# Kernel optimization log

Measured on AMD Instinct MI355X. Metric: run time of the kernel, lower is better.

## Reference

```python
import jax, jax.numpy as jnp
import numpy as np
from functools import partial

N = 50000
IN_C, HID_C, OUT_C = 256, 128, 64
E = 800000


def gcn_norm(src, dst, n_nodes):
    # PyG gcn_norm with unit edge weights: deg from target index, D^-1/2 A D^-1/2
    ones = jnp.ones(src.shape[0], dtype=jnp.float32)
    deg = jax.ops.segment_sum(ones, dst, num_segments=n_nodes)
    dinv = jnp.where(deg > 0, jax.lax.rsqrt(deg), 0.0)
    return dinv[src] * dinv[dst]


def gcn_conv(x, src, dst, norm, W, b):
    h = x @ W                              # [N, out] dense GEMM first (PyG order)
    msg = h[src] * norm[:, None]           # gather + scale  [E', out]
    out = jax.ops.segment_sum(msg, dst, num_segments=x.shape[0])
    return out + b


def setup_inputs() -> dict:
    key = jax.random.key(0)
    ks = jax.random.split(key, 6)
    x = jax.random.normal(ks[0], (N, IN_C), dtype=jnp.float32)
    edge_index = jax.random.randint(ks[1], (2, E), 0, N, dtype=jnp.int32)
    # Glorot-ish init for weights
    W1 = jax.random.normal(ks[2], (IN_C, HID_C), dtype=jnp.float32) / np.sqrt(IN_C)
    b1 = jnp.zeros((HID_C,), dtype=jnp.float32)
    W2 = jax.random.normal(ks[3], (HID_C, OUT_C), dtype=jnp.float32) / np.sqrt(HID_C)
    b2 = jnp.zeros((OUT_C,), dtype=jnp.float32)
    return {"x": x, "edge_index": edge_index, "W1": W1, "b1": b1, "W2": W2, "b2": b2}


def reference(x, edge_index, W1, b1, W2, b2):
    # eval mode: dropout is identity
    n = x.shape[0]
    loop = jnp.arange(n, dtype=edge_index.dtype)
    src = jnp.concatenate([edge_index[0], loop])   # add self loops (static E+N)
    dst = jnp.concatenate([edge_index[1], loop])
    norm = gcn_norm(src, dst, n)
    h = jax.nn.relu(gcn_conv(x, src, dst, norm, W1, b1))
    return gcn_conv(h, src, dst, norm, W2, b2)
```

## Files before the change

### kernel.cpp

```cpp
#include <hip/hip_runtime.h>


#define TPB 256
#define NBKT 196
#define EB_CAP 4608
#define CSR_CAP 6400
#define P1_EPB 4096

typedef __bf16 bf16x8 __attribute__((ext_vector_type(8)));
typedef __bf16 bf16x4 __attribute__((ext_vector_type(4)));
typedef __bf16 bf16x2 __attribute__((ext_vector_type(2)));
typedef float f32x4 __attribute__((ext_vector_type(4)));

__device__ __forceinline__ float bflo(unsigned u) { return __uint_as_float(u << 16); }
__device__ __forceinline__ float bfhi(unsigned u) { return __uint_as_float(u & 0xffff0000u); }

__global__ __launch_bounds__(256) void clear_wprep_kernel(
    unsigned* __restrict__ gcnt, float* __restrict__ dinv, __bf16* __restrict__ h2s,
    int N,
    const float* __restrict__ W1, const float* __restrict__ W2,
    __bf16* __restrict__ wf1, __bf16* __restrict__ wf2) {
    if (blockIdx.x == 0) {
        int t = threadIdx.x;
        if (t < NBKT) gcnt[t] = 0;
        if (t == 0) dinv[N] = 0.0f;
        if (t < 32) ((unsigned*)(h2s + (long)N * 64))[t] = 0u;
        return;
    }
    int g = (blockIdx.x - 1) * TPB + threadIdx.x;
    if (g < 64 * 64) {
        int frag = g >> 6, L = g & 63;
        int kstep = frag >> 3, oct = frag & 7;
        int oc = oct * 16 + (L & 15);
        int k0 = kstep * 32 + (L >> 4) * 8;
        bf16x8 v;
#pragma unroll
        for (int j = 0; j < 8; j++) v[j] = (__bf16)W1[(k0 + j) * 128 + oc];
        ((bf16x8*)wf1)[g] = v;
    } else if (g < 64 * 64 + 16 * 64) {
        int g2 = g - 64 * 64;
        int frag = g2 >> 6, L = g2 & 63;
        int kstep = frag >> 2, oct = frag & 3;
        int oc = oct * 16 + (L & 15);
        int k0 = kstep * 32 + (L >> 4) * 8;
        bf16x8 v;
#pragma unroll
        for (int j = 0; j < 8; j++) v[j] = (__bf16)W2[(k0 + j) * 64 + oc];
        ((bf16x8*)wf2)[g2] = v;
    }
}

__device__ __forceinline__ void gemm1_body(int bid, int tid, const float* __restrict__ x,
                                           const bf16x8* __restrict__ wfrag,
                                           __bf16* __restrict__ outp, int M) {
    int wave = tid >> 6, lane = tid & 63;
    int col = lane & 15, q = lane >> 4;
    long r0 = (long)bid * 64 + wave * 16 + col;
    long r0c = (r0 < M) ? r0 : (M - 1);

    f32x4 acc[8];
#pragma unroll
    for (int o = 0; o < 8; o++) acc[o] = (f32x4){0.f, 0.f, 0.f, 0.f};

#pragma unroll
    for (int ks = 0; ks < 8; ks++) {
        int k0 = ks * 32 + q * 8;
        const float* A0 = x + r0c * 256 + k0;
        float4 f0a = *(const float4*)A0;
        float4 f0b = *(const float4*)(A0 + 4);
        bf16x8 b0;
        b0[0] = (__bf16)f0a.x; b0[1] = (__bf16)f0a.y; b0[2] = (__bf16)f0a.z; b0[3] = (__bf16)f0a.w;
        b0[4] = (__bf16)f0b.x; b0[5] = (__bf16)f0b.y; b0[6] = (__bf16)f0b.z; b0[7] = (__bf16)f0b.w;
#pragma unroll
        for (int ot = 0; ot < 8; ot++) {
            bf16x8 a = wfrag[(ks * 8 + ot) * 64 + lane];
            acc[ot] = __builtin_amdgcn_mfma_f32_16x16x32_bf16(a, b0, acc[ot], 0, 0, 0);
        }
    }

    if (r0 < M) {
#pragma unroll
        for (int ot = 0; ot < 8; ot++) {
            int oc = ot * 16 + q * 4;
            bf16x4 v;
#pragma unroll
            for (int r = 0; r < 4; r++) v[r] = (__bf16)acc[ot][r];
            *(bf16x4*)(outp + r0 * 128 + oc) = v;
        }
    }
}

__global__ __launch_bounds__(256) void p1_gemm1_kernel(
    const int* __restrict__ src, const int* __restrict__ dst, int E, int p1Blocks,
    unsigned* __restrict__ gcnt, unsigned* __restrict__ ebuf,
    const float* __restrict__ x, const bf16x8* __restrict__ wf1,
    __bf16* __restrict__ h1u, int M) {
    __shared__ unsigned sPacked[P1_EPB];
    __shared__ int sCnt[256];
    if ((int)blockIdx.x < p1Blocks) {
        int t = threadIdx.x;
        sCnt[t] = 0;
        __syncthreads();
        long e0 = (long)blockIdx.x * P1_EPB;
        int cnt = (int)(E - e0);
        if (cnt > P1_EPB) cnt = P1_EPB;
        for (int i = t; i < cnt; i += 256) {
            unsigned s = (unsigned)src[e0 + i];
            unsigned d = (unsigned)dst[e0 + i];
            sPacked[i] = (s << 16) | d;
            atomicAdd(&sCnt[d >> 8], 1);
        }
        __syncthreads();
        int base = 0;
        if (t < NBKT) base = (int)atomicAdd(&gcnt[t], (unsigned)sCnt[t]);
        __syncthreads();
        if (t < NBKT) sCnt[t] = t * EB_CAP + base;
        __syncthreads();
        for (int i = t; i < cnt; i += 256) {
            unsigned p = sPacked[i];
            int b = (int)((p & 0xffffu) >> 8);
            int pos = atomicAdd(&sCnt[b], 1);
            if (pos < (b + 1) * EB_CAP) ebuf[pos] = p;
        }
    } else {
        gemm1_body(blockIdx.x - p1Blocks, threadIdx.x, x, wf1, h1u, M);
    }
}

__global__ __launch_bounds__(256) void csr_kernel(
    const unsigned* __restrict__ gcnt, const unsigned* __restrict__ ebuf,
    int* __restrict__ csr, int2* __restrict__ se, float* __restrict__ dinv, int N) {
    __shared__ unsigned sEdges[EB_CAP];
    __shared__ int sCnt[256];
    __shared__ int sScan[256];
    int b = blockIdx.x, t = threadIdx.x;
    int m = (int)gcnt[b];
    if (m > EB_CAP) m = EB_CAP;
    sCnt[t] = 0;
    __syncthreads();
    const unsigned* eb = ebuf + b * EB_CAP;
    for (int i = t; i < m; i += 256) {
        unsigned p = eb[i];
        sEdges[i] = p;
        atomicAdd(&sCnt[p & 255u], 1);
    }
    __syncthreads();
    int c = sCnt[t];
    int pad = (c + 7) & ~7;
    sScan[t] = pad;
    __syncthreads();
    for (int off = 1; off < 256; off <<= 1) {
        int v = (t >= off) ? sScan[t - off] : 0;
        __syncthreads();
        sScan[t] += v;
        __syncthreads();
    }
    int start = b * CSR_CAP + sScan[t] - pad;
    int node = (b << 8) + t;
    if (node < N) {
        se[node] = make_int2(start, start + pad);
        dinv[node] = rsqrtf((float)c + 1.0f);
    }
    __syncthreads();
    sCnt[t] = start;
    __syncthreads();
    for (int i = t; i < m; i += 256) {
        unsigned p = sEdges[i];
        int pos = atomicAdd(&sCnt[p & 255u], 1);
        csr[pos] = (int)(p >> 16);
    }
    if (node < N) {
        for (int k = start + c; k < start + pad; k++) csr[k] = N;
    }
}

#define ACC8()                                             \
    do {                                                   \
        a0x += bflo(v0) * w0; a0y += bfhi(v0) * w0;        \
        a1x += bflo(v1) * w1; a1y += bfhi(v1) * w1;        \
        a2x += bflo(v2) * w2; a2y += bfhi(v2) * w2;        \
        a3x += bflo(v3) * w3; a3y += bfhi(v3) * w3;        \
        a0x += bflo(v4) * w4; a0y += bfhi(v4) * w4;        \
        a1x += bflo(v5) * w5; a1y += bfhi(v5) * w5;        \
        a2x += bflo(v6) * w6; a2y += bfhi(v6) * w6;        \
        a3x += bflo(v7) * w7; a3y += bfhi(v7) * w7;        \
    } while (0)

__global__ __launch_bounds__(256) void agg128_gemm2_kernel(
    const __bf16* __restrict__ h, const int* __restrict__ csr,
    const int2* __restrict__ se, const float* __restrict__ dinv,
    const float* __restrict__ bias, const bf16x8* __restrict__ wf2,
    __bf16* __restrict__ h2s, int N) {
    __shared__ __bf16 stash[16 * 132];
    int wave = threadIdx.x >> 6, lane = threadIdx.x & 63;
    int n0 = blockIdx.x * 16;
    unsigned* stw = (unsigned*)stash;

    float2 bv = ((const float2*)bias)[lane];
#pragma unroll 1
    for (int i = 0; i < 4; i++) {
        int n = n0 + wave * 4 + i;
        float ox = 0.f, oy = 0.f;
        if (n < N) {
            int2 s_e = se[n];
            int start = s_e.x, m = s_e.y - s_e.x;
            float dn = dinv[n];
            const unsigned* hp = (const unsigned*)h;
            const int* sl = csr + start;
            unsigned self = hp[(long)n * 64 + lane];
            float a0x = bflo(self) * dn, a0y = bfhi(self) * dn;
            float a1x = 0.f, a1y = 0.f, a2x = 0.f, a2y = 0.f, a3x = 0.f, a3y = 0.f;
            if (m > 0) {
                int4 c0 = *(const int4*)sl;
                int4 c1 = *(const int4*)(sl + 4);
                int i0 = __builtin_amdgcn_readfirstlane(c0.x);
                int i1 = __builtin_amdgcn_readfirstlane(c0.y);
                int i2 = __builtin_amdgcn_readfirstlane(c0.z);
                int i3 = __builtin_amdgcn_readfirstlane(c0.w);
                int i4 = __builtin_amdgcn_readfirstlane(c1.x);
                int i5 = __builtin_amdgcn_readfirstlane(c1.y);
                int i6 = __builtin_amdgcn_readfirstlane(c1.z);
                int i7 = __builtin_amdgcn_readfirstlane(c1.w);
                unsigned v0 = hp[(long)i0 * 64 + lane], v1 = hp[(long)i1 * 64 + lane];
                unsigned v2 = hp[(long)i2 * 64 + lane], v3 = hp[(long)i3 * 64 + lane];
                unsigned v4 = hp[(long)i4 * 64 + lane], v5 = hp[(long)i5 * 64 + lane];
                unsigned v6 = hp[(long)i6 * 64 + lane], v7 = hp[(long)i7 * 64 + lane];
                float w0 = dinv[i0], w1 = dinv[i1], w2 = dinv[i2], w3 = dinv[i3];
                float w4 = dinv[i4], w5 = dinv[i5], w6 = dinv[i6], w7 = dinv[i7];
                int4 d0 = *(const int4*)(sl + 8);
                int4 d1 = *(const int4*)(sl + 12);
                for (int j = 8; j < m; j += 8) {
                    int t0 = __builtin_amdgcn_readfirstlane(d0.x);
                    int t1 = __builtin_amdgcn_readfirstlane(d0.y);
                    int t2 = __builtin_amdgcn_readfirstlane(d0.z);
                    int t3 = __builtin_amdgcn_readfirstlane(d0.w);
                    int t4 = __builtin_amdgcn_readfirstlane(d1.x);
                    int t5 = __builtin_amdgcn_readfirstlane(d1.y);
                    int t6 = __builtin_amdgcn_readfirstlane(d1.z);
                    int t7 = __builtin_amdgcn_readfirstlane(d1.w);
                    unsigned u0 = hp[(long)t0 * 64 + lane], u1 = hp[(long)t1 * 64 + lane];
                    unsigned u2 = hp[(long)t2 * 64 + lane], u3 = hp[(long)t3 * 64 + lane];
                    unsigned u4 = hp[(long)t4 * 64 + lane], u5 = hp[(long)t5 * 64 + lane];
                    unsigned u6 = hp[(long)t6 * 64 + lane], u7 = hp[(long)t7 * 64 + lane];
                    float q0 = dinv[t0], q1 = dinv[t1], q2 = dinv[t2], q3 = dinv[t3];
                    float q4 = dinv[t4], q5 = dinv[t5], q6 = dinv[t6], q7 = dinv[t7];
                    d0 = *(const int4*)(sl + j + 8);
                    d1 = *(const int4*)(sl + j + 12);
                    ACC8();
                    v0 = u0; v1 = u1; v2 = u2; v3 = u3; v4 = u4; v5 = u5; v6 = u6; v7 = u7;
                    w0 = q0; w1 = q1; w2 = q2; w3 = q3; w4 = q4; w5 = q5; w6 = q6; w7 = q7;
                }
                ACC8();
            }
            ox = fmaxf((a0x + a1x + a2x + a3x) * dn + bv.x, 0.f);
            oy = fmaxf((a0y + a1y + a2y + a3y) * dn + bv.y, 0.f);
        }
        bf16x2 st = {(__bf16)ox, (__bf16)oy};
        stw[(wave * 4 + i) * 66 + lane] = *(unsigned*)&st;
    }
    __syncthreads();

    int col = lane & 15, q = lane >> 4;
    const __bf16* srow = stash + col * 132;
    f32x4 acc = (f32x4){0.f, 0.f, 0.f, 0.f};
#pragma unroll
    for (int ks = 0; ks < 4; ks++) {
        bf16x8 bb = *(const bf16x8*)(srow + ks * 32 + q * 8);
        bf16x8 a = wf2[(ks * 4 + wave) * 64 + lane];
        acc = __builtin_amdgcn_mfma_f32_16x16x32_bf16(a, bb, acc, 0, 0, 0);
    }
    int node = n0 + col;
    if (node < N) {
        float dn2 = dinv[node];
        bf16x4 v;
#pragma unroll
        for (int r = 0; r < 4; r++) v[r] = (__bf16)(acc[r] * dn2);
        *(bf16x4*)(h2s + (long)node * 64 + (wave * 16 + q * 4)) = v;
    }
}
#undef ACC8

#define ACC8B()                                                                            \
    do {                                                                                   \
        a0 += __uint_as_float((unsigned)v0 << 16); a1 += __uint_as_float((unsigned)v1 << 16); \
        a2 += __uint_as_float((unsigned)v2 << 16); a3 += __uint_as_float((unsigned)v3 << 16); \
        a0 += __uint_as_float((unsigned)v4 << 16); a1 += __uint_as_float((unsigned)v5 << 16); \
        a2 += __uint_as_float((unsigned)v6 << 16); a3 += __uint_as_float((unsigned)v7 << 16); \
    } while (0)

__global__ __launch_bounds__(256) void agg64_kernel(const __bf16* __restrict__ hs,
                                                    const int* __restrict__ csr,
                                                    const int2* __restrict__ se,
                                                    const float* __restrict__ dinv,
                                                    const float* __restrict__ bias,
                                                    float* __restrict__ outp, int N) {
    int gid = blockIdx.x * TPB + threadIdx.x;
    int n = gid >> 6, lane = gid & 63;
    if (n >= N) return;
    int2 s_e = se[n];
    int start = s_e.x, m = s_e.y - s_e.x;
    float dn = dinv[n];
    const unsigned short* hp = (const unsigned short*)hs;
    const int* sl = csr + start;
    float a0 = __uint_as_float(((unsigned)hp[(long)n * 64 + lane]) << 16);
    float a1 = 0.f, a2 = 0.f, a3 = 0.f;
    if (m > 0) {
        int4 c0 = *(const int4*)sl;
        int4 c1 = *(const int4*)(sl + 4);
        int i0 = __builtin_amdgcn_readfirstlane(c0.x);
        int i1 = __builtin_amdgcn_readfirstlane(c0.y);
        int i2 = __builtin_amdgcn_readfirstlane(c0.z);
        int i3 = __builtin_amdgcn_readfirstlane(c0.w);
        int i4 = __builtin_amdgcn_readfirstlane(c1.x);
        int i5 = __builtin_amdgcn_readfirstlane(c1.y);
        int i6 = __builtin_amdgcn_readfirstlane(c1.z);
        int i7 = __builtin_amdgcn_readfirstlane(c1.w);
        unsigned short v0 = hp[(long)i0 * 64 + lane], v1 = hp[(long)i1 * 64 + lane];
        unsigned short v2 = hp[(long)i2 * 64 + lane], v3 = hp[(long)i3 * 64 + lane];
        unsigned short v4 = hp[(long)i4 * 64 + lane], v5 = hp[(long)i5 * 64 + lane];
        unsigned short v6 = hp[(long)i6 * 64 + lane], v7 = hp[(long)i7 * 64 + lane];
        int4 d0 = *(const int4*)(sl + 8);
        int4 d1 = *(const int4*)(sl + 12);
        for (int j = 8; j < m; j += 8) {
            int t0 = __builtin_amdgcn_readfirstlane(d0.x);
            int t1 = __builtin_amdgcn_readfirstlane(d0.y);
            int t2 = __builtin_amdgcn_readfirstlane(d0.z);
            int t3 = __builtin_amdgcn_readfirstlane(d0.w);
            int t4 = __builtin_amdgcn_readfirstlane(d1.x);
            int t5 = __builtin_amdgcn_readfirstlane(d1.y);
            int t6 = __builtin_amdgcn_readfirstlane(d1.z);
            int t7 = __builtin_amdgcn_readfirstlane(d1.w);
            unsigned short u0 = hp[(long)t0 * 64 + lane], u1 = hp[(long)t1 * 64 + lane];
            unsigned short u2 = hp[(long)t2 * 64 + lane], u3 = hp[(long)t3 * 64 + lane];
            unsigned short u4 = hp[(long)t4 * 64 + lane], u5 = hp[(long)t5 * 64 + lane];
            unsigned short u6 = hp[(long)t6 * 64 + lane], u7 = hp[(long)t7 * 64 + lane];
            d0 = *(const int4*)(sl + j + 8);
            d1 = *(const int4*)(sl + j + 12);
            ACC8B();
            v0 = u0; v1 = u1; v2 = u2; v3 = u3; v4 = u4; v5 = u5; v6 = u6; v7 = u7;
        }
        ACC8B();
    }
    outp[(long)n * 64 + lane] = (a0 + a1 + a2 + a3) * dn + bias[lane];
}
#undef ACC8B

static inline int cdiv(long a, long b) { return (int)((a + b - 1) / b); }

extern "C" void kernel_launch(void* const* d_in, const int* in_sizes, int n_in,
                              void* d_out, int out_size, void* d_ws, size_t ws_size,
                              hipStream_t stream) {
    const float* x  = (const float*)d_in[0];
    const int*   ei = (const int*)d_in[1];
    const float* W1 = (const float*)d_in[2];
    const float* b1 = (const float*)d_in[3];
    const float* W2 = (const float*)d_in[4];
    const float* b2 = (const float*)d_in[5];

    const int IN_C = 256;
    const int N = in_sizes[0] / IN_C;
    const int E = in_sizes[1] / 2;
    const int* src = ei;
    const int* dst = ei + E;

    char* w = (char*)d_ws;
    size_t off = 0;
    auto alloc = [&](size_t bytes) { void* p = w + off; off = (off + bytes + 255) & ~255ull; return p; };
    __bf16*   h1u  = (__bf16*)alloc((size_t)(N + 1) * 128 * 2);
    __bf16*   h2s  = (__bf16*)alloc((size_t)(N + 1) * 64 * 2);
    unsigned* ebuf = (unsigned*)alloc((size_t)NBKT * EB_CAP * 4);
    int*      csr  = (int*)alloc((size_t)NBKT * CSR_CAP * 4);
    int2*     se   = (int2*)alloc((size_t)N * 8);
    float*    dinv = (float*)alloc((size_t)(N + 1) * 4);
    unsigned* gcnt = (unsigned*)alloc(NBKT * 4);
    __bf16*   wf1  = (__bf16*)alloc(64 * 64 * 8 * 2);
    __bf16*   wf2  = (__bf16*)alloc(16 * 64 * 8 * 2);

    int wprepBlocks = cdiv(64 * 64 + 16 * 64, TPB);
    clear_wprep_kernel<<<1 + wprepBlocks, TPB, 0, stream>>>(gcnt, dinv, h2s, N,
                                                            W1, W2, wf1, wf2);

    int p1Blocks = cdiv(E, P1_EPB);
    int gemmBlocks = cdiv(N, 64);
    p1_gemm1_kernel<<<p1Blocks + gemmBlocks, TPB, 0, stream>>>(
        src, dst, E, p1Blocks, gcnt, ebuf, x, (const bf16x8*)wf1, h1u, N);

    csr_kernel<<<NBKT, TPB, 0, stream>>>(gcnt, ebuf, csr, se, dinv, N);

    agg128_gemm2_kernel<<<cdiv(N, 16), TPB, 0, stream>>>(h1u, csr, se, dinv, b1,
                                                         (const bf16x8*)wf2, h2s, N);

    agg64_kernel<<<cdiv((long)N * 64, TPB), TPB, 0, stream>>>(h2s, csr, se, dinv, b2,
                                                              (float*)d_out, N);
}
```

Baseline: 179.4 us.

## Gather neighbor rows with wide per-lane loads split across lane quarters

```diff
diff --git a/kernel.cpp b/kernel.cpp
--- a/kernel.cpp
+++ b/kernel.cpp
@@ -53,7 +53,8 @@
 __device__ __forceinline__ void gemm1_body(int bid, int tid, const float* __restrict__ x,
                                            const bf16x8* __restrict__ wfrag,
                                            __bf16* __restrict__ outp, int M) {
-    int wave = tid >> 6, lane = tid & 63;
+    int lane = tid & 63;
+    int wave = tid >> 6;
     int col = lane & 15, q = lane >> 4;
     long r0 = (long)bid * 64 + wave * 16 + col;
     long r0c = (r0 < M) ? r0 : (M - 1);
@@ -174,16 +175,12 @@
     }
 }
 
-#define ACC8()                                             \
-    do {                                                   \
-        a0x += bflo(v0) * w0; a0y += bfhi(v0) * w0;        \
-        a1x += bflo(v1) * w1; a1y += bfhi(v1) * w1;        \
-        a2x += bflo(v2) * w2; a2y += bfhi(v2) * w2;        \
-        a3x += bflo(v3) * w3; a3y += bfhi(v3) * w3;        \
-        a0x += bflo(v4) * w4; a0y += bfhi(v4) * w4;        \
-        a1x += bflo(v5) * w5; a1y += bfhi(v5) * w5;        \
-        a2x += bflo(v6) * w6; a2y += bfhi(v6) * w6;        \
-        a3x += bflo(v7) * w7; a3y += bfhi(v7) * w7;        \
+#define ACC8W(v, wgt)                                             \
+    do {                                                          \
+        acc0 += bflo((v).x) * (wgt); acc1 += bfhi((v).x) * (wgt); \
+        acc2 += bflo((v).y) * (wgt); acc3 += bfhi((v).y) * (wgt); \
+        acc4 += bflo((v).z) * (wgt); acc5 += bfhi((v).z) * (wgt); \
+        acc6 += bflo((v).w) * (wgt); acc7 += bfhi((v).w) * (wgt); \
     } while (0)
 
 __global__ __launch_bounds__(256) void agg128_gemm2_kernel(
@@ -194,69 +191,84 @@
     __shared__ __bf16 stash[16 * 132];
     int wave = threadIdx.x >> 6, lane = threadIdx.x & 63;
     int n0 = blockIdx.x * 16;
-    unsigned* stw = (unsigned*)stash;
-
-    float2 bv = ((const float2*)bias)[lane];
+    const char* hb = (const char*)h;
+    int l16 = lane & 15;
+    bool gb1 = (lane & 16) != 0, gb2 = (lane & 32) != 0;
+
+    float4 bv0 = ((const float4*)bias)[l16 * 2];
+    float4 bv1 = ((const float4*)bias)[l16 * 2 + 1];
+
 #pragma unroll 1
     for (int i = 0; i < 4; i++) {
         int n = n0 + wave * 4 + i;
-        float ox = 0.f, oy = 0.f;
+        float o0 = 0.f, o1 = 0.f, o2 = 0.f, o3 = 0.f, o4 = 0.f, o5 = 0.f, o6 = 0.f, o7 = 0.f;
         if (n < N) {
             int2 s_e = se[n];
             int start = s_e.x, m = s_e.y - s_e.x;
             float dn = dinv[n];
-            const unsigned* hp = (const unsigned*)h;
             const int* sl = csr + start;
-            unsigned self = hp[(long)n * 64 + lane];
-            float a0x = bflo(self) * dn, a0y = bfhi(self) * dn;
-            float a1x = 0.f, a1y = 0.f, a2x = 0.f, a2y = 0.f, a3x = 0.f, a3y = 0.f;
+            float selfw = (lane < 16) ? dn : 0.f;
+            uint4 vs = *(const uint4*)(hb + (long)n * 256 + l16 * 16);
+            float acc0 = bflo(vs.x) * selfw, acc1 = bfhi(vs.x) * selfw;
+            float acc2 = bflo(vs.y) * selfw, acc3 = bfhi(vs.y) * selfw;
+            float acc4 = bflo(vs.z) * selfw, acc5 = bfhi(vs.z) * selfw;
+            float acc6 = bflo(vs.w) * selfw, acc7 = bfhi(vs.w) * selfw;
             if (m > 0) {
                 int4 c0 = *(const int4*)sl;
                 int4 c1 = *(const int4*)(sl + 4);
-                int i0 = __builtin_amdgcn_readfirstlane(c0.x);
-                int i1 = __builtin_amdgcn_readfirstlane(c0.y);
-                int i2 = __builtin_amdgcn_readfirstlane(c0.z);
-                int i3 = __builtin_amdgcn_readfirstlane(c0.w);
-                int i4 = __builtin_amdgcn_readfirstlane(c1.x);
-                int i5 = __builtin_amdgcn_readfirstlane(c1.y);
-                int i6 = __builtin_amdgcn_readfirstlane(c1.z);
-                int i7 = __builtin_amdgcn_readfirstlane(c1.w);
-                unsigned v0 = hp[(long)i0 * 64 + lane], v1 = hp[(long)i1 * 64 + lane];
-                unsigned v2 = hp[(long)i2 * 64 + lane], v3 = hp[(long)i3 * 64 + lane];
-                unsigned v4 = hp[(long)i4 * 64 + lane], v5 = hp[(long)i5 * 64 + lane];
-                unsigned v6 = hp[(long)i6 * 64 + lane], v7 = hp[(long)i7 * 64 + lane];
-                float w0 = dinv[i0], w1 = dinv[i1], w2 = dinv[i2], w3 = dinv[i3];
-                float w4 = dinv[i4], w5 = dinv[i5], w6 = dinv[i6], w7 = dinv[i7];
+                int t01 = gb1 ? c0.y : c0.x;
+                int t23 = gb1 ? c0.w : c0.z;
+                int ia = gb2 ? t23 : t01;
+                t01 = gb1 ? c1.y : c1.x;
+                t23 = gb1 ? c1.w : c1.z;
+                int ib = gb2 ? t23 : t01;
+                uint4 va = *(const uint4*)(hb + (long)ia * 256 + l16 * 16);
+                uint4 vb = *(const uint4*)(hb + (long)ib * 256 + l16 * 16);
+                float wa = dinv[ia], wb = dinv[ib];
                 int4 d0 = *(const int4*)(sl + 8);
                 int4 d1 = *(const int4*)(sl + 12);
                 for (int j = 8; j < m; j += 8) {
-                    int t0 = __builtin_amdgcn_readfirstlane(d0.x);
-                    int t1 = __builtin_amdgcn_readfirstlane(d0.y);
-                    int t2 = __builtin_amdgcn_readfirstlane(d0.z);
-                    int t3 = __builtin_amdgcn_readfirstlane(d0.w);
-                    int t4 = __builtin_amdgcn_readfirstlane(d1.x);
-                    int t5 = __builtin_amdgcn_readfirstlane(d1.y);
-                    int t6 = __builtin_amdgcn_readfirstlane(d1.z);
-                    int t7 = __builtin_amdgcn_readfirstlane(d1.w);
-                    unsigned u0 = hp[(long)t0 * 64 + lane], u1 = hp[(long)t1 * 64 + lane];
-                    unsigned u2 = hp[(long)t2 * 64 + lane], u3 = hp[(long)t3 * 64 + lane];
-                    unsigned u4 = hp[(long)t4 * 64 + lane], u5 = hp[(long)t5 * 64 + lane];
-                    unsigned u6 = hp[(long)t6 * 64 + lane], u7 = hp[(long)t7 * 64 + lane];
-                    float q0 = dinv[t0], q1 = dinv[t1], q2 = dinv[t2], q3 = dinv[t3];
-                    float q4 = dinv[t4], q5 = dinv[t5], q6 = dinv[t6], q7 = dinv[t7];
+                    int s01 = gb1 ? d0.y : d0.x;
+                    int s23 = gb1 ? d0.w : d0.z;
+                    int na = gb2 ? s23 : s01;
+                    s01 = gb1 ? d1.y : d1.x;
+                    s23 = gb1 ? d1.w : d1.z;
+                    int nb = gb2 ? s23 : s01;
+                    uint4 ua = *(const uint4*)(hb + (long)na * 256 + l16 * 16);
+                    uint4 ub = *(const uint4*)(hb + (long)nb * 256 + l16 * 16);
+                    float qa = dinv[na], qb = dinv[nb];
                     d0 = *(const int4*)(sl + j + 8);
                     d1 = *(const int4*)(sl + j + 12);
-                    ACC8();
-                    v0 = u0; v1 = u1; v2 = u2; v3 = u3; v4 = u4; v5 = u5; v6 = u6; v7 = u7;
-                    w0 = q0; w1 = q1; w2 = q2; w3 = q3; w4 = q4; w5 = q5; w6 = q6; w7 = q7;
+                    ACC8W(va, wa);
+                    ACC8W(vb, wb);
+                    va = ua; vb = ub; wa = qa; wb = qb;
                 }
-                ACC8();
+                ACC8W(va, wa);
+                ACC8W(vb, wb);
             }
-            ox = fmaxf((a0x + a1x + a2x + a3x) * dn + bv.x, 0.f);
-            oy = fmaxf((a0y + a1y + a2y + a3y) * dn + bv.y, 0.f);
-        }
-        bf16x2 st = {(__bf16)ox, (__bf16)oy};
-        stw[(wave * 4 + i) * 66 + lane] = *(unsigned*)&st;
+            acc0 += __shfl_xor(acc0, 16); acc0 += __shfl_xor(acc0, 32);
+            acc1 += __shfl_xor(acc1, 16); acc1 += __shfl_xor(acc1, 32);
+            acc2 += __shfl_xor(acc2, 16); acc2 += __shfl_xor(acc2, 32);
+            acc3 += __shfl_xor(acc3, 16); acc3 += __shfl_xor(acc3, 32);
+            acc4 += __shfl_xor(acc4, 16); acc4 += __shfl_xor(acc4, 32);
+            acc5 += __shfl_xor(acc5, 16); acc5 += __shfl_xor(acc5, 32);
+            acc6 += __shfl_xor(acc6, 16); acc6 += __shfl_xor(acc6, 32);
+            acc7 += __shfl_xor(acc7, 16); acc7 += __shfl_xor(acc7, 32);
+            o0 = fmaxf(acc0 * dn + bv0.x, 0.f);
+            o1 = fmaxf(acc1 * dn + bv0.y, 0.f);
+            o2 = fmaxf(acc2 * dn + bv0.z, 0.f);
+            o3 = fmaxf(acc3 * dn + bv0.w, 0.f);
+            o4 = fmaxf(acc4 * dn + bv1.x, 0.f);
+            o5 = fmaxf(acc5 * dn + bv1.y, 0.f);
+            o6 = fmaxf(acc6 * dn + bv1.z, 0.f);
+            o7 = fmaxf(acc7 * dn + bv1.w, 0.f);
+        }
+        if (lane < 16) {
+            bf16x8 st;
+            st[0] = (__bf16)o0; st[1] = (__bf16)o1; st[2] = (__bf16)o2; st[3] = (__bf16)o3;
+            st[4] = (__bf16)o4; st[5] = (__bf16)o5; st[6] = (__bf16)o6; st[7] = (__bf16)o7;
+            *(bf16x8*)(stash + (wave * 4 + i) * 132 + l16 * 8) = st;
+        }
     }
     __syncthreads();
 
@@ -278,14 +290,12 @@
         *(bf16x4*)(h2s + (long)node * 64 + (wave * 16 + q * 4)) = v;
     }
 }
-#undef ACC8
-
-#define ACC8B()                                                                            \
-    do {                                                                                   \
-        a0 += __uint_as_float((unsigned)v0 << 16); a1 += __uint_as_float((unsigned)v1 << 16); \
-        a2 += __uint_as_float((unsigned)v2 << 16); a3 += __uint_as_float((unsigned)v3 << 16); \
-        a0 += __uint_as_float((unsigned)v4 << 16); a1 += __uint_as_float((unsigned)v5 << 16); \
-        a2 += __uint_as_float((unsigned)v6 << 16); a3 += __uint_as_float((unsigned)v7 << 16); \
+#undef ACC8W
+
+#define ACC4W(v)                                           \
+    do {                                                   \
+        acc0 += bflo((v).x); acc1 += bfhi((v).x);          \
+        acc2 += bflo((v).y); acc3 += bfhi((v).y);          \
     } while (0)
 
 __global__ __launch_bounds__(256) void agg64_kernel(const __bf16* __restrict__ hs,
@@ -300,50 +310,61 @@
     int2 s_e = se[n];
     int start = s_e.x, m = s_e.y - s_e.x;
     float dn = dinv[n];
-    const unsigned short* hp = (const unsigned short*)hs;
+    const char* hb = (const char*)hs;
     const int* sl = csr + start;
-    float a0 = __uint_as_float(((unsigned)hp[(long)n * 64 + lane]) << 16);
-    float a1 = 0.f, a2 = 0.f, a3 = 0.f;
+    int l16 = lane & 15;
+    bool gb1 = (lane & 16) != 0, gb2 = (lane & 32) != 0;
+
+    float selfw = (lane < 16) ? 1.f : 0.f;
+    uint2 vs = *(const uint2*)(hb + (long)n * 128 + l16 * 8);
+    float acc0 = bflo(vs.x) * selfw, acc1 = bfhi(vs.x) * selfw;
+    float acc2 = bflo(vs.y) * selfw, acc3 = bfhi(vs.y) * selfw;
     if (m > 0) {
         int4 c0 = *(const int4*)sl;
         int4 c1 = *(const int4*)(sl + 4);
-        int i0 = __builtin_amdgcn_readfirstlane(c0.x);
-        int i1 = __builtin_amdgcn_readfirstlane(c0.y);
-        int i2 = __builtin_amdgcn_readfirstlane(c0.z);
-        int i3 = __builtin_amdgcn_readfirstlane(c0.w);
-        int i4 = __builtin_amdgcn_readfirstlane(c1.x);
-        int i5 = __builtin_amdgcn_readfirstlane(c1.y);
-        int i6 = __builtin_amdgcn_readfirstlane(c1.z);
-        int i7 = __builtin_amdgcn_readfirstlane(c1.w);
-        unsigned short v0 = hp[(long)i0 * 64 + lane], v1 = hp[(long)i1 * 64 + lane];
-        unsigned short v2 = hp[(long)i2 * 64 + lane], v3 = hp[(long)i3 * 64 + lane];
-        unsigned short v4 = hp[(long)i4 * 64 + lane], v5 = hp[(long)i5 * 64 + lane];
-        unsigned short v6 = hp[(long)i6 * 64 + lane], v7 = hp[(long)i7 * 64 + lane];
+        int t01 = gb1 ? c0.y : c0.x;
+        int t23 = gb1 ? c0.w : c0.z;
+        int ia = gb2 ? t23 : t01;
+        t01 = gb1 ? c1.y : c1.x;
+        t23 = gb1 ? c1.w : c1.z;
+        int ib = gb2 ? t23 : t01;
+        uint2 va = *(const uint2*)(hb + (long)ia * 128 + l16 * 8);
+        uint2 vb = *(const uint2*)(hb + (long)ib * 128 + l16 * 8);
         int4 d0 = *(const int4*)(sl + 8);
         int4 d1 = *(const int4*)(sl + 12);
         for (int j = 8; j < m; j += 8) {
-            int t0 = __builtin_amdgcn_readfirstlane(d0.x);
-            int t1 = __builtin_amdgcn_readfirstlane(d0.y);
-            int t2 = __builtin_amdgcn_readfirstlane(d0.z);
-            int t3 = __builtin_amdgcn_readfirstlane(d0.w);
-            int t4 = __builtin_amdgcn_readfirstlane(d1.x);
-            int t5 = __builtin_amdgcn_readfirstlane(d1.y);
-            int t6 = __builtin_amdgcn_readfirstlane(d1.z);
-            int t7 = __builtin_amdgcn_readfirstlane(d1.w);
-            unsigned short u0 = hp[(long)t0 * 64 + lane], u1 = hp[(long)t1 * 64 + lane];
-            unsigned short u2 = hp[(long)t2 * 64 + lane], u3 = hp[(long)t3 * 64 + lane];
-            unsigned short u4 = hp[(long)t4 * 64 + lane], u5 = hp[(long)t5 * 64 + lane];
-            unsigned short u6 = hp[(long)t6 * 64 + lane], u7 = hp[(long)t7 * 64 + lane];
+            int s01 = gb1 ? d0.y : d0.x;
+            int s23 = gb1 ? d0.w : d0.z;
+            int na = gb2 ? s23 : s01;
+            s01 = gb1 ? d1.y : d1.x;
+            s23 = gb1 ? d1.w : d1.z;
+            int nb = gb2 ? s23 : s01;
+            uint2 ua = *(const uint2*)(hb + (long)na * 128 + l16 * 8);
+            uint2 ub = *(const uint2*)(hb + (long)nb * 128 + l16 * 8);
             d0 = *(const int4*)(sl + j + 8);
             d1 = *(const int4*)(sl + j + 12);
-            ACC8B();
-            v0 = u0; v1 = u1; v2 = u2; v3 = u3; v4 = u4; v5 = u5; v6 = u6; v7 = u7;
-        }
-        ACC8B();
-    }
-    outp[(long)n * 64 + lane] = (a0 + a1 + a2 + a3) * dn + bias[lane];
-}
-#undef ACC8B
+            ACC4W(va);
+            ACC4W(vb);
+            va = ua; vb = ub;
+        }
+        ACC4W(va);
+        ACC4W(vb);
+    }
+    acc0 += __shfl_xor(acc0, 16); acc0 += __shfl_xor(acc0, 32);
+    acc1 += __shfl_xor(acc1, 16); acc1 += __shfl_xor(acc1, 32);
+    acc2 += __shfl_xor(acc2, 16); acc2 += __shfl_xor(acc2, 32);
+    acc3 += __shfl_xor(acc3, 16); acc3 += __shfl_xor(acc3, 32);
+    if (lane < 16) {
+        float4 bv = ((const float4*)bias)[l16];
+        float4 o;
+        o.x = acc0 * dn + bv.x;
+        o.y = acc1 * dn + bv.y;
+        o.z = acc2 * dn + bv.z;
+        o.w = acc3 * dn + bv.w;
+        ((float4*)(outp + (long)n * 64))[l16] = o;
+    }
+}
+#undef ACC4W
 
 static inline int cdiv(long a, long b) { return (int)((a + b - 1) / b); }
 
```

Measured after the change: 184.2 us. 1.03x slower.

## Replace global-atomic bucketing with per-block local sort and fuse CSR build with GEMM1

Applied to the files above, without the earlier changes.

```diff
diff --git a/kernel.cpp b/kernel.cpp
--- a/kernel.cpp
+++ b/kernel.cpp
@@ -3,9 +3,10 @@
 
 #define TPB 256
 #define NBKT 196
+#define P1_BLKS 196
+#define P1_EPB 4096
 #define EB_CAP 4608
 #define CSR_CAP 6400
-#define P1_EPB 4096
 
 typedef __bf16 bf16x8 __attribute__((ext_vector_type(8)));
 typedef __bf16 bf16x4 __attribute__((ext_vector_type(4)));
@@ -15,45 +16,90 @@
 __device__ __forceinline__ float bflo(unsigned u) { return __uint_as_float(u << 16); }
 __device__ __forceinline__ float bfhi(unsigned u) { return __uint_as_float(u & 0xffff0000u); }
 
-__global__ __launch_bounds__(256) void clear_wprep_kernel(
-    unsigned* __restrict__ gcnt, float* __restrict__ dinv, __bf16* __restrict__ h2s,
-    int N,
+__global__ __launch_bounds__(256) void p1_pack_kernel(
+    const int* __restrict__ src, const int* __restrict__ dst, int E,
+    unsigned* __restrict__ gcnt2, unsigned* __restrict__ boffs2,
+    unsigned* __restrict__ ebuf,
     const float* __restrict__ W1, const float* __restrict__ W2,
-    __bf16* __restrict__ wf1, __bf16* __restrict__ wf2) {
-    if (blockIdx.x == 0) {
-        int t = threadIdx.x;
-        if (t < NBKT) gcnt[t] = 0;
-        if (t == 0) dinv[N] = 0.0f;
-        if (t < 32) ((unsigned*)(h2s + (long)N * 64))[t] = 0u;
+    __bf16* __restrict__ wf1, __bf16* __restrict__ wf2,
+    float* __restrict__ dinv, __bf16* __restrict__ h2s, int N) {
+    __shared__ unsigned sPacked[P1_EPB];
+    __shared__ int sCnt[256];
+    __shared__ int sScan[256];
+    int bx = (int)blockIdx.x, t = threadIdx.x;
+    if (bx < P1_BLKS) {
+        sCnt[t] = 0;
+        __syncthreads();
+        long e0 = (long)bx * P1_EPB;
+        int cnt = (int)(E - e0);
+        if (cnt > P1_EPB) cnt = P1_EPB;
+        if (cnt < 0) cnt = 0;
+        for (int i = t; i < cnt; i += 256) {
+            unsigned s = (unsigned)src[e0 + i];
+            unsigned d = (unsigned)dst[e0 + i];
+            sPacked[i] = (s << 16) | d;
+            atomicAdd(&sCnt[d >> 8], 1);
+        }
+        __syncthreads();
+        int c = sCnt[t];
+        sScan[t] = c;
+        __syncthreads();
+        for (int off = 1; off < 256; off <<= 1) {
+            int v = (t >= off) ? sScan[t - off] : 0;
+            __syncthreads();
+            sScan[t] += v;
+            __syncthreads();
+        }
+        int boff = sScan[t] - c;
+        if (t < NBKT) {
+            gcnt2[bx * NBKT + t] = (unsigned)c;
+            boffs2[bx * NBKT + t] = (unsigned)boff;
+        }
+        __syncthreads();
+        sCnt[t] = boff;
+        __syncthreads();
+        unsigned* myout = ebuf + (long)bx * P1_EPB;
+        for (int i = t; i < cnt; i += 256) {
+            unsigned p = sPacked[i];
+            int b = (int)((p & 0xffffu) >> 8);
+            int pos = atomicAdd(&sCnt[b], 1);
+            myout[pos] = p;
+        }
         return;
     }
-    int g = (blockIdx.x - 1) * TPB + threadIdx.x;
-    if (g < 64 * 64) {
-        int frag = g >> 6, L = g & 63;
-        int kstep = frag >> 3, oct = frag & 7;
-        int oc = oct * 16 + (L & 15);
-        int k0 = kstep * 32 + (L >> 4) * 8;
-        bf16x8 v;
-#pragma unroll
-        for (int j = 0; j < 8; j++) v[j] = (__bf16)W1[(k0 + j) * 128 + oc];
-        ((bf16x8*)wf1)[g] = v;
-    } else if (g < 64 * 64 + 16 * 64) {
-        int g2 = g - 64 * 64;
-        int frag = g2 >> 6, L = g2 & 63;
-        int kstep = frag >> 2, oct = frag & 3;
-        int oc = oct * 16 + (L & 15);
-        int k0 = kstep * 32 + (L >> 4) * 8;
-        bf16x8 v;
-#pragma unroll
-        for (int j = 0; j < 8; j++) v[j] = (__bf16)W2[(k0 + j) * 64 + oc];
-        ((bf16x8*)wf2)[g2] = v;
-    }
+    if (bx < P1_BLKS + 20) {
+        int g = (bx - P1_BLKS) * TPB + t;
+        if (g < 64 * 64) {
+            int frag = g >> 6, L = g & 63;
+            int kstep = frag >> 3, oct = frag & 7;
+            int oc = oct * 16 + (L & 15);
+            int k0 = kstep * 32 + (L >> 4) * 8;
+            bf16x8 v;
+#pragma unroll
+            for (int j = 0; j < 8; j++) v[j] = (__bf16)W1[(k0 + j) * 128 + oc];
+            ((bf16x8*)wf1)[g] = v;
+        } else if (g < 64 * 64 + 16 * 64) {
+            int g2 = g - 64 * 64;
+            int frag = g2 >> 6, L = g2 & 63;
+            int kstep = frag >> 2, oct = frag & 3;
+            int oc = oct * 16 + (L & 15);
+            int k0 = kstep * 32 + (L >> 4) * 8;
+            bf16x8 v;
+#pragma unroll
+            for (int j = 0; j < 8; j++) v[j] = (__bf16)W2[(k0 + j) * 64 + oc];
+            ((bf16x8*)wf2)[g2] = v;
+        }
+        return;
+    }
+    if (t == 0) dinv[N] = 0.0f;
+    if (t < 32) ((unsigned*)(h2s + (long)N * 64))[t] = 0u;
 }
 
 __device__ __forceinline__ void gemm1_body(int bid, int tid, const float* __restrict__ x,
                                            const bf16x8* __restrict__ wfrag,
                                            __bf16* __restrict__ outp, int M) {
-    int wave = tid >> 6, lane = tid & 63;
+    int lane = tid & 63;
+    int wave = tid >> 6;
     int col = lane & 15, q = lane >> 4;
     long r0 = (long)bid * 64 + wave * 16 + col;
     long r0c = (r0 < M) ? r0 : (M - 1);
@@ -90,61 +136,39 @@
     }
 }
 
-__global__ __launch_bounds__(256) void p1_gemm1_kernel(
-    const int* __restrict__ src, const int* __restrict__ dst, int E, int p1Blocks,
-    unsigned* __restrict__ gcnt, unsigned* __restrict__ ebuf,
+__global__ __launch_bounds__(256) void csr_gemm1_kernel(
+    const unsigned* __restrict__ gcnt2, const unsigned* __restrict__ boffs2,
+    const unsigned* __restrict__ ebuf,
+    int* __restrict__ csr, int2* __restrict__ se, float* __restrict__ dinv, int N,
     const float* __restrict__ x, const bf16x8* __restrict__ wf1,
-    __bf16* __restrict__ h1u, int M) {
-    __shared__ unsigned sPacked[P1_EPB];
-    __shared__ int sCnt[256];
-    if ((int)blockIdx.x < p1Blocks) {
-        int t = threadIdx.x;
-        sCnt[t] = 0;
-        __syncthreads();
-        long e0 = (long)blockIdx.x * P1_EPB;
-        int cnt = (int)(E - e0);
-        if (cnt > P1_EPB) cnt = P1_EPB;
-        for (int i = t; i < cnt; i += 256) {
-            unsigned s = (unsigned)src[e0 + i];
-            unsigned d = (unsigned)dst[e0 + i];
-            sPacked[i] = (s << 16) | d;
-            atomicAdd(&sCnt[d >> 8], 1);
-        }
-        __syncthreads();
-        int base = 0;
-        if (t < NBKT) base = (int)atomicAdd(&gcnt[t], (unsigned)sCnt[t]);
-        __syncthreads();
-        if (t < NBKT) sCnt[t] = t * EB_CAP + base;
-        __syncthreads();
-        for (int i = t; i < cnt; i += 256) {
-            unsigned p = sPacked[i];
-            int b = (int)((p & 0xffffu) >> 8);
-            int pos = atomicAdd(&sCnt[b], 1);
-            if (pos < (b + 1) * EB_CAP) ebuf[pos] = p;
-        }
-    } else {
-        gemm1_body(blockIdx.x - p1Blocks, threadIdx.x, x, wf1, h1u, M);
-    }
-}
-
-__global__ __launch_bounds__(256) void csr_kernel(
-    const unsigned* __restrict__ gcnt, const unsigned* __restrict__ ebuf,
-    int* __restrict__ csr, int2* __restrict__ se, float* __restrict__ dinv, int N) {
+    __bf16* __restrict__ h1u) {
     __shared__ unsigned sEdges[EB_CAP];
     __shared__ int sCnt[256];
     __shared__ int sScan[256];
-    int b = blockIdx.x, t = threadIdx.x;
-    int m = (int)gcnt[b];
+    __shared__ int sTot;
+    int b = (int)blockIdx.x, t = threadIdx.x;
+    if (b >= NBKT) {
+        gemm1_body(b - NBKT, t, x, wf1, h1u, N);
+        return;
+    }
+    sCnt[t] = 0;
+    if (t == 0) sTot = 0;
+    __syncthreads();
+    if (t < P1_BLKS) {
+        int c = (int)gcnt2[t * NBKT + b];
+        int off = (int)boffs2[t * NBKT + b];
+        int pos = atomicAdd(&sTot, c);
+        const unsigned* chunk = ebuf + (long)t * P1_EPB + off;
+        for (int i = 0; i < c; i++) {
+            if (pos + i >= EB_CAP) break;
+            unsigned p = chunk[i];
+            sEdges[pos + i] = p;
+            atomicAdd(&sCnt[p & 255u], 1);
+        }
+    }
+    __syncthreads();
+    int m = sTot;
     if (m > EB_CAP) m = EB_CAP;
-    sCnt[t] = 0;
-    __syncthreads();
-    const unsigned* eb = ebuf + b * EB_CAP;
-    for (int i = t; i < m; i += 256) {
-        unsigned p = eb[i];
-        sEdges[i] = p;
-        atomicAdd(&sCnt[p & 255u], 1);
-    }
-    __syncthreads();
     int c = sCnt[t];
     int pad = (c + 7) & ~7;
     sScan[t] = pad;
@@ -366,26 +390,23 @@
     char* w = (char*)d_ws;
     size_t off = 0;
     auto alloc = [&](size_t bytes) { void* p = w + off; off = (off + bytes + 255) & ~255ull; return p; };
-    __bf16*   h1u  = (__bf16*)alloc((size_t)(N + 1) * 128 * 2);
-    __bf16*   h2s  = (__bf16*)alloc((size_t)(N + 1) * 64 * 2);
-    unsigned* ebuf = (unsigned*)alloc((size_t)NBKT * EB_CAP * 4);
-    int*      csr  = (int*)alloc((size_t)NBKT * CSR_CAP * 4);
-    int2*     se   = (int2*)alloc((size_t)N * 8);
-    float*    dinv = (float*)alloc((size_t)(N + 1) * 4);
-    unsigned* gcnt = (unsigned*)alloc(NBKT * 4);
-    __bf16*   wf1  = (__bf16*)alloc(64 * 64 * 8 * 2);
-    __bf16*   wf2  = (__bf16*)alloc(16 * 64 * 8 * 2);
-
-    int wprepBlocks = cdiv(64 * 64 + 16 * 64, TPB);
-    clear_wprep_kernel<<<1 + wprepBlocks, TPB, 0, stream>>>(gcnt, dinv, h2s, N,
-                                                            W1, W2, wf1, wf2);
-
-    int p1Blocks = cdiv(E, P1_EPB);
+    __bf16*   h1u    = (__bf16*)alloc((size_t)(N + 1) * 128 * 2);
+    __bf16*   h2s    = (__bf16*)alloc((size_t)(N + 1) * 64 * 2);
+    unsigned* ebuf   = (unsigned*)alloc((size_t)P1_BLKS * P1_EPB * 4);
+    int*      csr    = (int*)alloc((size_t)NBKT * CSR_CAP * 4);
+    int2*     se     = (int2*)alloc((size_t)N * 8);
+    float*    dinv   = (float*)alloc((size_t)(N + 1) * 4);
+    unsigned* gcnt2  = (unsigned*)alloc((size_t)P1_BLKS * NBKT * 4);
+    unsigned* boffs2 = (unsigned*)alloc((size_t)P1_BLKS * NBKT * 4);
+    __bf16*   wf1    = (__bf16*)alloc(64 * 64 * 8 * 2);
+    __bf16*   wf2    = (__bf16*)alloc(16 * 64 * 8 * 2);
+
+    p1_pack_kernel<<<P1_BLKS + 20 + 1, TPB, 0, stream>>>(
+        src, dst, E, gcnt2, boffs2, ebuf, W1, W2, wf1, wf2, dinv, h2s, N);
+
     int gemmBlocks = cdiv(N, 64);
-    p1_gemm1_kernel<<<p1Blocks + gemmBlocks, TPB, 0, stream>>>(
-        src, dst, E, p1Blocks, gcnt, ebuf, x, (const bf16x8*)wf1, h1u, N);
-
-    csr_kernel<<<NBKT, TPB, 0, stream>>>(gcnt, ebuf, csr, se, dinv, N);
+    csr_gemm1_kernel<<<NBKT + gemmBlocks, TPB, 0, stream>>>(
+        gcnt2, boffs2, ebuf, csr, se, dinv, N, x, (const bf16x8*)wf1, h1u);
 
     agg128_gemm2_kernel<<<cdiv(N, 16), TPB, 0, stream>>>(h1u, csr, se, dinv, b1,
                                                          (const bf16x8*)wf2, h2s, N);
```

Measured after the change: 182.7 us. About the same (+1.9%).
